# Performance work log

Measured on AMD Instinct MI355X. Metric: run time of the kernel, lower is better.

## Reference

```python
import jax, jax.numpy as jnp
import numpy as np
from jax import lax

T = 100
TAU = 2.0
ALPHA = 2.0  # ATan surrogate default
EPS = 1e-5

@jax.custom_vjp
def atan_spike(x):
    return (x >= 0.0).astype(x.dtype)

def _atan_fwd(x):
    return atan_spike(x), x

def _atan_bwd(x, g):
    return (g * (ALPHA / 2.0) / (1.0 + (jnp.pi / 2.0 * ALPHA * x) ** 2),)

atan_spike.defvjp(_atan_fwd, _atan_bwd)

def lif(x_seq):
    # spikingjelly LIFNode: decay_input=True, v_threshold=1, hard reset to 0
    def step(v, x):
        v = v + (x - v) / TAU
        s = atan_spike(v - 1.0)
        return v * (1.0 - s), s
    return lax.scan(step, jnp.zeros_like(x_seq[0]), x_seq)[1]

def conv3x3(x, w):
    return lax.conv_general_dilated(x, w, (1, 1), 'SAME',
                                    dimension_numbers=('NCHW', 'OIHW', 'NCHW'))

def bn(x, g, b, m, v):
    inv = g / jnp.sqrt(v + EPS)
    return x * inv[:, None, None] + (b - m * inv)[:, None, None]

def maxpool2(x):
    return lax.reduce_window(x, -jnp.inf, lax.max, (1, 1, 2, 2), (1, 1, 2, 2), 'VALID')

def setup_inputs() -> dict:
    key = jax.random.key(0)
    ks = jax.random.split(key, 10)
    B, C = 16, 64
    x = jax.random.uniform(ks[0], (B, 1, 28, 28), dtype=jnp.float32)
    W1 = jax.random.normal(ks[1], (C, 1, 3, 3), dtype=jnp.float32) * np.sqrt(2.0 / 9)
    W2 = jax.random.normal(ks[2], (C, C, 3, 3), dtype=jnp.float32) * np.sqrt(2.0 / (9 * C))
    Wfc1 = jax.random.normal(ks[3], (C * 16, C * 49), dtype=jnp.float32) * np.sqrt(2.0 / (C * 49))
    Wfc2 = jax.random.normal(ks[4], (10, C * 16), dtype=jnp.float32) * np.sqrt(2.0 / (C * 16))
    g1 = jnp.ones((C,), jnp.float32); b1 = jnp.zeros((C,), jnp.float32)
    m1 = jax.random.normal(ks[5], (C,), jnp.float32) * 0.1
    v1 = jax.random.uniform(ks[6], (C,), jnp.float32, 0.5, 1.5)
    g2 = jnp.ones((C,), jnp.float32); b2 = jnp.zeros((C,), jnp.float32)
    m2 = jax.random.normal(ks[7], (C,), jnp.float32) * 0.1
    v2 = jax.random.uniform(ks[8], (C,), jnp.float32, 0.5, 1.5)
    return {'x': x, 'W1': W1, 'g1': g1, 'b1': b1, 'm1': m1, 'v1': v1,
            'W2': W2, 'g2': g2, 'b2': b2, 'm2': m2, 'v2': v2,
            'Wfc1': Wfc1, 'Wfc2': Wfc2}

def reference(x, W1, g1, b1, m1, v1, W2, g2, b2, m2, v2, Wfc1, Wfc2):
    B = x.shape[0]
    C = W1.shape[0]
    # conv1+BN1: input identical at every timestep, compute once and broadcast
    h1 = bn(conv3x3(x, W1), g1, b1, m1, v1)                 # [B,C,28,28]
    x_seq = jnp.broadcast_to(h1, (T,) + h1.shape)           # [T,B,C,28,28]
    s1 = lif(x_seq)                                         # [T,B,C,28,28]
    p1 = maxpool2(s1.reshape(T * B, C, 28, 28))             # [T*B,C,14,14]
    h2 = bn(conv3x3(p1, W2), g2, b2, m2, v2).reshape(T, B, C, 14, 14)
    s2 = lif(h2)                                            # [T,B,C,14,14]
    p2 = maxpool2(s2.reshape(T * B, C, 14, 14)).reshape(T, B, C * 49)
    s3 = lif(jnp.einsum('tbi,oi->tbo', p2, Wfc1))           # [T,B,C*16]
    s4 = lif(jnp.einsum('tbi,oi->tbo', s3, Wfc2))           # [T,B,10]
    return s4.mean(axis=0)                                  # [B,10]
```

## Files before the change

### kernel.cpp

```cpp
#include <hip/hip_runtime.h>
#include <hip/hip_bf16.h>

typedef unsigned int uint;
typedef _Float16 f16;
typedef _Float16 f16x8 __attribute__((ext_vector_type(8)));
typedef float f32x4 __attribute__((ext_vector_type(4)));

#define T_STEPS 100

#define OFF_H1    (size_t)0
#define OFF_WHI   (size_t)0
#define OFF_WLO   (size_t)73728
#define OFF_P1    (size_t)3211264
#define OFF_H2    (size_t)29425664
#define OFF_H3    (size_t)29425664
#define OFF_S3    (size_t)35979264
#define OFF_H4    (size_t)37617664
#define OFF_WF1L  (size_t)37681664
#define OFF_WF1H  (size_t)44104192
#define OFF_P2H   (size_t)109707264

__device__ __forceinline__ int lif_step_i(float& v, float x) {
  v = __fadd_rn(v, __fmul_rn(__fsub_rn(x, v), 0.5f));
  if (v >= 1.0f) { v = 0.0f; return 1; }
  return 0;
}

__global__ __launch_bounds__(256) void k_prep_w2(const float* __restrict__ w2,
                                                 f16* __restrict__ whi, f16* __restrict__ wlo) {
  int i = blockIdx.x * 256 + threadIdx.x;
  int j = i & 7, l = (i >> 3) & 63, cb = (i >> 9) & 3, kb = i >> 11;
  int k = kb * 32 + (l >> 4) * 8 + j;
  int co = cb * 16 + (l & 15);
  int ci = k & 63, tap = k >> 6;
  int dy = tap / 3, dx = tap - 3 * dy;
  float w = w2[((co * 64 + ci) * 3 + dy) * 3 + dx];
  float hif = (fabsf(w) < 6.104e-5f) ? 0.0f : (float)(f16)w;
  whi[i] = (f16)hif;
  wlo[i] = (f16)((w - hif) * 4096.0f);
}

__global__ __launch_bounds__(256) void k_prep_wfc1(const float* __restrict__ wfc1,
                                                   f16* __restrict__ whi, f16* __restrict__ wlo) {
  int i = blockIdx.x * 256 + threadIdx.x;
  int j = i & 7, lane = (i >> 3) & 63;
  int rest = i >> 9;
  int oblk = rest & 63, kbG = rest >> 6;
  int o = oblk * 16 + (lane & 15);
  int k = kbG * 32 + (lane >> 4) * 8 + j;
  float w = wfc1[(size_t)o * 3136 + k];
  float hif = (fabsf(w) < 6.104e-5f) ? 0.0f : (float)(f16)w;
  whi[i] = (f16)hif;
  wlo[i] = (f16)((w - hif) * 4096.0f);
}

__global__ __launch_bounds__(256) void k_zero_h3(float4* __restrict__ p) {
  p[blockIdx.x * 256 + threadIdx.x] = make_float4(0.f, 0.f, 0.f, 0.f);
}

__global__ __launch_bounds__(256) void k_conv1(const float* __restrict__ x, const float* __restrict__ w1,
                                               const float* __restrict__ g1, const float* __restrict__ b1,
                                               const float* __restrict__ m1, const float* __restrict__ v1,
                                               float* __restrict__ h1) {
  int i = blockIdx.x * 256 + threadIdx.x;
  int pos = i % 784;
  int bc  = i / 784;
  int c = bc & 63, b = bc >> 6;
  int y = pos / 28, xx = pos % 28;
  float a = 0.f;
#pragma unroll
  for (int dy = 0; dy < 3; ++dy) {
    int iy = y + dy - 1;
#pragma unroll
    for (int dx = 0; dx < 3; ++dx) {
      int ix = xx + dx - 1;
      if (iy >= 0 && iy < 28 && ix >= 0 && ix < 28)
        a = fmaf(w1[c * 9 + dy * 3 + dx], x[b * 784 + iy * 28 + ix], a);
    }
  }
  float inv  = g1[c] / sqrtf(v1[c] + 1e-5f);
  float bias = __fsub_rn(b1[c], __fmul_rn(m1[c], inv));
  h1[i] = __fadd_rn(__fmul_rn(a, inv), bias);
}

__global__ __launch_bounds__(256) void k_lif1pool(const float* __restrict__ h1,
                                                  unsigned char* __restrict__ p1) {
  int t = blockIdx.x * 256 + threadIdx.x;
  int ci = t & 63, xx = (t >> 6) & 15, y = (t >> 10) & 15, b = t >> 14;
  int pix = y * 16 + xx;
  size_t outbase = (size_t)b * 16384 + pix * 64 + ci;
  const size_t tstride = (size_t)16 * 16384;
  if (y == 0 || y == 15 || xx == 0 || xx == 15) {
    for (int tt = 0; tt < T_STEPS; ++tt) p1[outbase + (size_t)tt * tstride] = 0;
    return;
  }
  int py = y - 1, px = xx - 1;
  const float* hp = h1 + ((size_t)(b * 64 + ci) * 28 + 2 * py) * 28 + 2 * px;
  float h00 = hp[0], h01 = hp[1], h10 = hp[28], h11 = hp[29];
  float v00 = 0.f, v01 = 0.f, v10 = 0.f, v11 = 0.f;
  for (int tt = 0; tt < T_STEPS; ++tt) {
    int s = 0;
    s |= lif_step_i(v00, h00);
    s |= lif_step_i(v01, h01);
    s |= lif_step_i(v10, h10);
    s |= lif_step_i(v11, h11);
    p1[outbase + (size_t)tt * tstride] = (unsigned char)s;
  }
}

__global__ __launch_bounds__(256, 2) void k_conv2(const unsigned char* __restrict__ p1,
                                                  const f16* __restrict__ whi, const f16* __restrict__ wlo,
                                                  const float* __restrict__ g2, const float* __restrict__ b2,
                                                  const float* __restrict__ m2, const float* __restrict__ v2,
                                                  float* __restrict__ h2) {
  __shared__ unsigned char smem[33024];
  const int tid = threadIdx.x;
  const int tb = blockIdx.x;
  const unsigned char* img = p1 + (size_t)tb * 16384;
#pragma unroll
  for (int it = 0; it < 4; ++it) {
    int s = it * 256 + tid;
    uint4 d = *(const uint4*)(img + (size_t)s * 16);
    int pix = s >> 2, c4 = s & 3;
    uint dw[4] = {d.x, d.y, d.z, d.w};
    f16x8 va, vb;
#pragma unroll
    for (int e = 0; e < 8; ++e) {
      va[e] = (f16)(float)((dw[e >> 2] >> ((e & 3) * 8)) & 255u);
      vb[e] = (f16)(float)((dw[2 + (e >> 2)] >> ((e & 3) * 8)) & 255u);
    }
    int rowbase = pix * 128;
    int sw = (pix & 7) << 4;
    *(f16x8*)(smem + rowbase + ((c4 * 32) ^ sw)) = va;
    *(f16x8*)(smem + rowbase + ((c4 * 32 + 16) ^ sw)) = vb;
  }
  if (tid < 16) *(uint4*)(smem + 32768 + tid * 16) = make_uint4(0u, 0u, 0u, 0u);
  __syncthreads();

  const int lane = tid & 63;
  const int wave = tid >> 6;
  const int ox = lane & 15;
  const int g = lane >> 4;
  const int cohalf = wave & 1;
  const int pb0 = (wave >> 1) * 7;

  f32x4 aH0[7], aL0[7], aH1[7], aL1[7];
#pragma unroll
  for (int q = 0; q < 7; ++q) {
    aH0[q] = (f32x4){0.f, 0.f, 0.f, 0.f};
    aL0[q] = (f32x4){0.f, 0.f, 0.f, 0.f};
    aH1[q] = (f32x4){0.f, 0.f, 0.f, 0.f};
    aL1[q] = (f32x4){0.f, 0.f, 0.f, 0.f};
  }

#pragma unroll 2
  for (int kb = 0; kb < 18; ++kb) {
    const int tap = kb >> 1;
    const int dy = tap / 3, dx = tap - 3 * dy;
    const int cilo2 = (kb & 1) * 64;
    size_t abase = ((size_t)(kb * 4 + cohalf * 2) * 64 + lane) * 8;
    f16x8 ah0 = *(const f16x8*)(whi + abase);
    f16x8 al0 = *(const f16x8*)(wlo + abase);
    f16x8 ah1 = *(const f16x8*)(whi + abase + 512);
    f16x8 al1 = *(const f16x8*)(wlo + abase + 512);
#pragma unroll
    for (int q = 0; q < 7; ++q) {
      int pix = (pb0 + q + dy) * 16 + ox + dx;
      int boff = pix * 128 + ((cilo2 + g * 16) ^ ((pix & 7) << 4));
      f16x8 bf = *(const f16x8*)(smem + boff);
      aH0[q] = __builtin_amdgcn_mfma_f32_16x16x32_f16(ah0, bf, aH0[q], 0, 0, 0);
      aL0[q] = __builtin_amdgcn_mfma_f32_16x16x32_f16(al0, bf, aL0[q], 0, 0, 0);
      aH1[q] = __builtin_amdgcn_mfma_f32_16x16x32_f16(ah1, bf, aH1[q], 0, 0, 0);
      aL1[q] = __builtin_amdgcn_mfma_f32_16x16x32_f16(al1, bf, aL1[q], 0, 0, 0);
    }
  }

  float binv[2][4], bofs[2][4];
#pragma unroll
  for (int cb = 0; cb < 2; ++cb)
#pragma unroll
    for (int r = 0; r < 4; ++r) {
      int co = (cohalf * 2 + cb) * 16 + g * 4 + r;
      float iv = g2[co] / sqrtf(v2[co] + 1e-5f);
      binv[cb][r] = iv;
      bofs[cb][r] = __fsub_rn(b2[co], __fmul_rn(m2[co], iv));
    }

  if (ox < 14) {
#pragma unroll
    for (int q = 0; q < 7; ++q) {
      int oy = pb0 + q;
#pragma unroll
      for (int r = 0; r < 4; ++r) {
        int co0 = cohalf * 32 + g * 4 + r;
        float s0 = __fadd_rn(aH0[q][r], __fmul_rn(aL0[q][r], 1.0f / 4096.0f));
        h2[((size_t)tb * 64 + co0) * 196 + oy * 14 + ox] =
            __fadd_rn(__fmul_rn(s0, binv[0][r]), bofs[0][r]);
        int co1 = co0 + 16;
        float s1 = __fadd_rn(aH1[q][r], __fmul_rn(aL1[q][r], 1.0f / 4096.0f));
        h2[((size_t)tb * 64 + co1) * 196 + oy * 14 + ox] =
            __fadd_rn(__fmul_rn(s1, binv[1][r]), bofs[1][r]);
      }
    }
  }
}

__global__ __launch_bounds__(256) void k_lif2pool(const float* __restrict__ h2,
                                                  f16* __restrict__ p2h) {
  int t = blockIdx.x * 256 + threadIdx.x;
  int px = t % 7;
  int r1 = t / 7;
  int py = r1 % 7;
  int r2 = r1 / 7;
  int c = r2 & 63, b = r2 >> 6;
  const float* base = h2 + ((size_t)b * 64 + c) * 196 + (2 * py) * 14 + 2 * px;
  const size_t tstride = (size_t)16 * 64 * 196;
  f16* op = p2h + (size_t)b * 3136 + c * 49 + py * 7 + px;
  const size_t otstride = (size_t)16 * 3136;
  float v00 = 0.f, v01 = 0.f, v10 = 0.f, v11 = 0.f;
#pragma unroll 4
  for (int tt = 0; tt < T_STEPS; ++tt) {
    const float* hp = base + (size_t)tt * tstride;
    float2 r0 = *(const float2*)(hp);
    float2 r1v = *(const float2*)(hp + 14);
    int s = 0;
    s |= lif_step_i(v00, r0.x);
    s |= lif_step_i(v01, r0.y);
    s |= lif_step_i(v10, r1v.x);
    s |= lif_step_i(v11, r1v.y);
    op[(size_t)tt * otstride] = (f16)s;
  }
}

__global__ __launch_bounds__(256, 3) void k_fc1(const f16* __restrict__ p2h,
                                                const f16* __restrict__ whi, const f16* __restrict__ wlo,
                                                float* __restrict__ h3) {
  __shared__ unsigned char bsm[2][128 * 80];
  const int tid = threadIdx.x;
  const int lane = tid & 63;
  const int wave = tid >> 6;
  int bid = blockIdx.x;
  int k8 = bid & 7, j = bid >> 3;
  int sh = j / 13, xb = j - sh * 13;
  int s = k8 + 8 * sh;
  int yb = s >> 1, z = s & 1;
  const int tb0 = xb * 128;
  const int oblk = yb * 4 + wave;
  const int tbl = tid >> 1, half = tid & 1;
  const int stb = tb0 + tbl;
  const bool sok = (stb < 1600);
  const uint4* spq = (const uint4*)(p2h + (size_t)stb * 3136 + z * 1568 + half * 16);

  f32x4 accH[8], accL[8];
#pragma unroll
  for (int n = 0; n < 8; ++n) {
    accH[n] = (f32x4){0.f, 0.f, 0.f, 0.f};
    accL[n] = (f32x4){0.f, 0.f, 0.f, 0.f};
  }

  const int kbG0 = z * 49;
  size_t afrag = ((size_t)(kbG0 * 64 + oblk) * 64 + lane) * 8;
  const size_t astep = (size_t)64 * 64 * 8;
  f16x8 ahC = *(const f16x8*)(whi + afrag);
  f16x8 alC = *(const f16x8*)(wlo + afrag);
  const uint4 z4 = make_uint4(0u, 0u, 0u, 0u);
  uint4 dA = sok ? spq[0] : z4;
  uint4 dB = sok ? spq[1] : z4;

  for (int kb = 0; kb < 49; ++kb) {
    uint4 nA = z4, nB = z4;
    f16x8 ahN = ahC, alN = alC;
    if (kb < 48) {
      if (sok) { nA = spq[kb * 4 + 4]; nB = spq[kb * 4 + 5]; }
      ahN = *(const f16x8*)(whi + afrag + (size_t)(kb + 1) * astep);
      alN = *(const f16x8*)(wlo + afrag + (size_t)(kb + 1) * astep);
    }
    unsigned char* row = &bsm[kb & 1][tbl * 80 + half * 32];
    *(uint4*)(row) = dA;
    *(uint4*)(row + 16) = dB;
    __syncthreads();
    const unsigned char* buf = &bsm[kb & 1][0];
#pragma unroll
    for (int n = 0; n < 8; ++n) {
      f16x8 bf = *(const f16x8*)(buf + (n * 16 + (lane & 15)) * 80 + (lane >> 4) * 16);
      accH[n] = __builtin_amdgcn_mfma_f32_16x16x32_f16(ahC, bf, accH[n], 0, 0, 0);
      accL[n] = __builtin_amdgcn_mfma_f32_16x16x32_f16(alC, bf, accL[n], 0, 0, 0);
    }
    dA = nA; dB = nB; ahC = ahN; alC = alN;
  }

  const int o = yb * 64 + wave * 16 + (lane >> 4) * 4;
#pragma unroll
  for (int n = 0; n < 8; ++n) {
    int tb = tb0 + n * 16 + (lane & 15);
    if (tb < 1600) {
      float* hp = h3 + (size_t)tb * 1024 + o;
#pragma unroll
      for (int r = 0; r < 4; ++r) {
        float sv = __fadd_rn(accH[n][r], __fmul_rn(accL[n][r], 1.0f / 4096.0f));
        atomicAdd(hp + r, sv);
      }
    }
  }
}

__global__ __launch_bounds__(256) void k_lif3(const float* __restrict__ h3,
                                              unsigned char* __restrict__ s3) {
  int t = blockIdx.x * 256 + threadIdx.x;
  int o = t & 1023, b = t >> 10;
  size_t base = (size_t)b * 1024 + o;
  float v = 0.f;
#pragma unroll 10
  for (int tt = 0; tt < T_STEPS; ++tt) {
    float xv = h3[base + (size_t)tt * 16384];
    s3[base + (size_t)tt * 16384] = (unsigned char)lif_step_i(v, xv);
  }
}

__global__ __launch_bounds__(64) void k_fc2(const unsigned char* __restrict__ s3,
                                            const float* __restrict__ wfc2,
                                            float* __restrict__ h4) {
  int tb = blockIdx.x;
  int l = threadIdx.x;
  const unsigned char* srow = s3 + (size_t)tb * 1024;
  float p[10];
#pragma unroll
  for (int o = 0; o < 10; ++o) p[o] = 0.f;
  for (int j = 0; j < 16; ++j) {
    int k = l + j * 64;
    float s = (float)srow[k];
#pragma unroll
    for (int o = 0; o < 10; ++o)
      p[o] = fmaf(s, wfc2[o * 1024 + k], p[o]);
  }
#pragma unroll
  for (int o = 0; o < 10; ++o) {
    float v = p[o];
    for (int off = 32; off > 0; off >>= 1) v += __shfl_down(v, off, 64);
    if (l == 0) h4[(size_t)tb * 10 + o] = v;
  }
}

__global__ __launch_bounds__(256) void k_lif4mean(const float* __restrict__ h4,
                                                  float* __restrict__ out) {
  int t = threadIdx.x;
  if (t >= 160) return;
  int o = t % 10, b = t / 10;
  float v = 0.f;
  int cnt = 0;
#pragma unroll 10
  for (int tt = 0; tt < T_STEPS; ++tt) {
    float xv = h4[(size_t)tt * 160 + b * 10 + o];
    cnt += lif_step_i(v, xv);
  }
  out[b * 10 + o] = (float)cnt / 100.0f;
}

extern "C" void kernel_launch(void* const* d_in, const int* in_sizes, int n_in,
                              void* d_out, int out_size, void* d_ws, size_t ws_size,
                              hipStream_t stream) {
  const float* x    = (const float*)d_in[0];
  const float* W1   = (const float*)d_in[1];
  const float* g1   = (const float*)d_in[2];
  const float* b1   = (const float*)d_in[3];
  const float* m1   = (const float*)d_in[4];
  const float* v1   = (const float*)d_in[5];
  const float* W2   = (const float*)d_in[6];
  const float* g2   = (const float*)d_in[7];
  const float* b2   = (const float*)d_in[8];
  const float* m2   = (const float*)d_in[9];
  const float* v2   = (const float*)d_in[10];
  const float* Wfc1 = (const float*)d_in[11];
  const float* Wfc2 = (const float*)d_in[12];
  float* out = (float*)d_out;
  char* ws = (char*)d_ws;

  float*         h1   = (float*)(ws + OFF_H1);
  f16*           whi  = (f16*)(ws + OFF_WHI);
  f16*           wlo  = (f16*)(ws + OFF_WLO);
  unsigned char* p1   = (unsigned char*)(ws + OFF_P1);
  float*         h2   = (float*)(ws + OFF_H2);
  f16*           p2h  = (f16*)(ws + OFF_P2H);
  float*         h3   = (float*)(ws + OFF_H3);
  unsigned char* s3   = (unsigned char*)(ws + OFF_S3);
  float*         h4   = (float*)(ws + OFF_H4);
  f16*           wf1h = (f16*)(ws + OFF_WF1H);
  f16*           wf1l = (f16*)(ws + OFF_WF1L);

  k_conv1<<<3136, 256, 0, stream>>>(x, W1, g1, b1, m1, v1, h1);
  k_lif1pool<<<1024, 256, 0, stream>>>(h1, p1);
  k_prep_w2<<<144, 256, 0, stream>>>(W2, whi, wlo);
  k_conv2<<<1600, 256, 0, stream>>>(p1, whi, wlo, g2, b2, m2, v2, h2);
  k_lif2pool<<<196, 256, 0, stream>>>(h2, p2h);
  k_prep_wfc1<<<12544, 256, 0, stream>>>(Wfc1, wf1h, wf1l);
  k_zero_h3<<<1600, 256, 0, stream>>>((float4*)h3);
  k_fc1<<<416, 256, 0, stream>>>(p2h, wf1h, wf1l, h3);
  k_lif3<<<64, 256, 0, stream>>>(h3, s3);
  k_fc2<<<1600, 64, 0, stream>>>(s3, Wfc2, h4);
  k_lif4mean<<<1, 256, 0, stream>>>(h4, out);
}
```

Baseline: 280.3 us.

## Replace fc1 split-K atomics with two partial buffers summed in lif3

The fc1 kernel now writes each K-half's partial sums with plain float4 stores into separate buffers (h3a/h3b) instead of atomically accumulating into a zeroed h3. The zeroing kernel is removed, and lif3 adds the two partials before the LIF step. The time-batch tile shrinks from 128 to 64 rows, which doubles the grid to 800 blocks, raises the occupancy hint to 4, and removes the bounds check. This removes atomic traffic and one launch, at the cost of an extra 6.5MB buffer that lif3 must read.

```diff
diff --git a/kernel.cpp b/kernel.cpp
--- a/kernel.cpp
+++ b/kernel.cpp
@@ -13,11 +13,12 @@
 #define OFF_WLO   (size_t)73728
 #define OFF_P1    (size_t)3211264
 #define OFF_H2    (size_t)29425664
-#define OFF_H3    (size_t)29425664
-#define OFF_S3    (size_t)35979264
-#define OFF_H4    (size_t)37617664
-#define OFF_WF1L  (size_t)37681664
-#define OFF_WF1H  (size_t)44104192
+#define OFF_H3A   (size_t)29425664
+#define OFF_H3B   (size_t)35979264
+#define OFF_S3    (size_t)42532864
+#define OFF_H4    (size_t)44171264
+#define OFF_WF1L  (size_t)44235264
+#define OFF_WF1H  (size_t)50657792
 #define OFF_P2H   (size_t)109707264
 
 __device__ __forceinline__ int lif_step_i(float& v, float x) {
@@ -52,10 +53,6 @@
   float hif = (fabsf(w) < 6.104e-5f) ? 0.0f : (float)(f16)w;
   whi[i] = (f16)hif;
   wlo[i] = (f16)((w - hif) * 4096.0f);
-}
-
-__global__ __launch_bounds__(256) void k_zero_h3(float4* __restrict__ p) {
-  p[blockIdx.x * 256 + threadIdx.x] = make_float4(0.f, 0.f, 0.f, 0.f);
 }
 
 __global__ __launch_bounds__(256) void k_conv1(const float* __restrict__ x, const float* __restrict__ w1,
@@ -232,88 +229,81 @@
   }
 }
 
-__global__ __launch_bounds__(256, 3) void k_fc1(const f16* __restrict__ p2h,
+__global__ __launch_bounds__(256, 4) void k_fc1(const f16* __restrict__ p2h,
                                                 const f16* __restrict__ whi, const f16* __restrict__ wlo,
-                                                float* __restrict__ h3) {
-  __shared__ unsigned char bsm[2][128 * 80];
+                                                float* __restrict__ h3a, float* __restrict__ h3b) {
+  __shared__ unsigned char bsm[2][64 * 80];
   const int tid = threadIdx.x;
   const int lane = tid & 63;
   const int wave = tid >> 6;
   int bid = blockIdx.x;
   int k8 = bid & 7, j = bid >> 3;
-  int sh = j / 13, xb = j - sh * 13;
+  int sh = j / 25, xb = j - sh * 25;
   int s = k8 + 8 * sh;
   int yb = s >> 1, z = s & 1;
-  const int tb0 = xb * 128;
+  const int tb0 = xb * 64;
   const int oblk = yb * 4 + wave;
-  const int tbl = tid >> 1, half = tid & 1;
-  const int stb = tb0 + tbl;
-  const bool sok = (stb < 1600);
-  const uint4* spq = (const uint4*)(p2h + (size_t)stb * 3136 + z * 1568 + half * 16);
-
-  f32x4 accH[8], accL[8];
-#pragma unroll
-  for (int n = 0; n < 8; ++n) {
+  const int tbl = tid >> 2, quarter = tid & 3;
+  const uint4* spq = (const uint4*)(p2h + (size_t)(tb0 + tbl) * 3136 + z * 1568 + quarter * 8);
+
+  f32x4 accH[4], accL[4];
+#pragma unroll
+  for (int n = 0; n < 4; ++n) {
     accH[n] = (f32x4){0.f, 0.f, 0.f, 0.f};
     accL[n] = (f32x4){0.f, 0.f, 0.f, 0.f};
   }
 
-  const int kbG0 = z * 49;
-  size_t afrag = ((size_t)(kbG0 * 64 + oblk) * 64 + lane) * 8;
+  size_t afrag = ((size_t)((z * 49) * 64 + oblk) * 64 + lane) * 8;
   const size_t astep = (size_t)64 * 64 * 8;
   f16x8 ahC = *(const f16x8*)(whi + afrag);
   f16x8 alC = *(const f16x8*)(wlo + afrag);
-  const uint4 z4 = make_uint4(0u, 0u, 0u, 0u);
-  uint4 dA = sok ? spq[0] : z4;
-  uint4 dB = sok ? spq[1] : z4;
+  uint4 dC = spq[0];
 
   for (int kb = 0; kb < 49; ++kb) {
-    uint4 nA = z4, nB = z4;
+    uint4 nC = dC;
     f16x8 ahN = ahC, alN = alC;
     if (kb < 48) {
-      if (sok) { nA = spq[kb * 4 + 4]; nB = spq[kb * 4 + 5]; }
+      nC = spq[kb * 4 + 4];
       ahN = *(const f16x8*)(whi + afrag + (size_t)(kb + 1) * astep);
       alN = *(const f16x8*)(wlo + afrag + (size_t)(kb + 1) * astep);
     }
-    unsigned char* row = &bsm[kb & 1][tbl * 80 + half * 32];
-    *(uint4*)(row) = dA;
-    *(uint4*)(row + 16) = dB;
+    *(uint4*)(&bsm[kb & 1][tbl * 80 + quarter * 16]) = dC;
     __syncthreads();
     const unsigned char* buf = &bsm[kb & 1][0];
 #pragma unroll
-    for (int n = 0; n < 8; ++n) {
+    for (int n = 0; n < 4; ++n) {
       f16x8 bf = *(const f16x8*)(buf + (n * 16 + (lane & 15)) * 80 + (lane >> 4) * 16);
       accH[n] = __builtin_amdgcn_mfma_f32_16x16x32_f16(ahC, bf, accH[n], 0, 0, 0);
       accL[n] = __builtin_amdgcn_mfma_f32_16x16x32_f16(alC, bf, accL[n], 0, 0, 0);
     }
-    dA = nA; dB = nB; ahC = ahN; alC = alN;
-  }
-
+    dC = nC; ahC = ahN; alC = alN;
+  }
+
+  float* h3z = z ? h3b : h3a;
   const int o = yb * 64 + wave * 16 + (lane >> 4) * 4;
 #pragma unroll
-  for (int n = 0; n < 8; ++n) {
+  for (int n = 0; n < 4; ++n) {
     int tb = tb0 + n * 16 + (lane & 15);
-    if (tb < 1600) {
-      float* hp = h3 + (size_t)tb * 1024 + o;
-#pragma unroll
-      for (int r = 0; r < 4; ++r) {
-        float sv = __fadd_rn(accH[n][r], __fmul_rn(accL[n][r], 1.0f / 4096.0f));
-        atomicAdd(hp + r, sv);
-      }
-    }
-  }
-}
-
-__global__ __launch_bounds__(256) void k_lif3(const float* __restrict__ h3,
+    float4 sv;
+    sv.x = __fadd_rn(accH[n][0], __fmul_rn(accL[n][0], 1.0f / 4096.0f));
+    sv.y = __fadd_rn(accH[n][1], __fmul_rn(accL[n][1], 1.0f / 4096.0f));
+    sv.z = __fadd_rn(accH[n][2], __fmul_rn(accL[n][2], 1.0f / 4096.0f));
+    sv.w = __fadd_rn(accH[n][3], __fmul_rn(accL[n][3], 1.0f / 4096.0f));
+    *(float4*)(h3z + (size_t)tb * 1024 + o) = sv;
+  }
+}
+
+__global__ __launch_bounds__(256) void k_lif3(const float* __restrict__ h3a,
+                                              const float* __restrict__ h3b,
                                               unsigned char* __restrict__ s3) {
   int t = blockIdx.x * 256 + threadIdx.x;
-  int o = t & 1023, b = t >> 10;
-  size_t base = (size_t)b * 1024 + o;
+  size_t base = (size_t)t;
   float v = 0.f;
 #pragma unroll 10
   for (int tt = 0; tt < T_STEPS; ++tt) {
-    float xv = h3[base + (size_t)tt * 16384];
-    s3[base + (size_t)tt * 16384] = (unsigned char)lif_step_i(v, xv);
+    size_t idx = base + (size_t)tt * 16384;
+    float xv = __fadd_rn(h3a[idx], h3b[idx]);
+    s3[idx] = (unsigned char)lif_step_i(v, xv);
   }
 }
 
@@ -381,7 +371,8 @@
   unsigned char* p1   = (unsigned char*)(ws + OFF_P1);
   float*         h2   = (float*)(ws + OFF_H2);
   f16*           p2h  = (f16*)(ws + OFF_P2H);
-  float*         h3   = (float*)(ws + OFF_H3);
+  float*         h3a  = (float*)(ws + OFF_H3A);
+  float*         h3b  = (float*)(ws + OFF_H3B);
   unsigned char* s3   = (unsigned char*)(ws + OFF_S3);
   float*         h4   = (float*)(ws + OFF_H4);
   f16*           wf1h = (f16*)(ws + OFF_WF1H);
@@ -393,9 +384,8 @@
   k_conv2<<<1600, 256, 0, stream>>>(p1, whi, wlo, g2, b2, m2, v2, h2);
   k_lif2pool<<<196, 256, 0, stream>>>(h2, p2h);
   k_prep_wfc1<<<12544, 256, 0, stream>>>(Wfc1, wf1h, wf1l);
-  k_zero_h3<<<1600, 256, 0, stream>>>((float4*)h3);
-  k_fc1<<<416, 256, 0, stream>>>(p2h, wf1h, wf1l, h3);
-  k_lif3<<<64, 256, 0, stream>>>(h3, s3);
+  k_fc1<<<800, 256, 0, stream>>>(p2h, wf1h, wf1l, h3a, h3b);
+  k_lif3<<<64, 256, 0, stream>>>(h3a, h3b, s3);
   k_fc2<<<1600, 64, 0, stream>>>(s3, Wfc2, h4);
   k_lif4mean<<<1, 256, 0, stream>>>(h4, out);
 }
```

Result: faster. 231.2 us (-17.5%).
